# Kernel optimization log

Measured on AMD Instinct MI355X. Metric: run time of the kernel, lower is better.

The kernel has to match this reference:

```python
import jax, jax.numpy as jnp
import numpy as np

V, K, H, B = 50000, 50, 300, 512
C_WEIGHTS = 0.0005
C_TOPICS = 5e-06
BN_EPS = 1e-5


def _bn(x, g, b, m, v):
    # eval-mode BatchNorm1d with running stats
    return (x - m) * jax.lax.rsqrt(v + BN_EPS) * g + b


def setup_inputs() -> dict:
    key = jax.random.key(0)
    ks = jax.random.split(key, 16)
    s = 0.02
    inp = {
        "bows": jax.random.uniform(ks[0], (B, V), jnp.float32),
        "normalized_bows": jax.random.uniform(ks[1], (B, V), jnp.float32),
        "labels": jax.random.normal(ks[2], (B,), jnp.float32),
        # encoder q_theta: Linear(V,H) -> relu -> BN -> Linear(H,H) -> relu -> BN
        "W1": jax.random.normal(ks[3], (H, V), jnp.float32) * s,
        "b1": jnp.zeros((H,), jnp.float32),
        "W2": jax.random.normal(ks[4], (H, H), jnp.float32) * s,
        "b2": jnp.zeros((H,), jnp.float32),
        "bn1_g": jnp.ones((H,), jnp.float32),
        "bn1_b": jnp.zeros((H,), jnp.float32),
        "bn1_m": jnp.zeros((H,), jnp.float32),
        "bn1_v": jnp.ones((H,), jnp.float32),
        "bn2_g": jnp.ones((H,), jnp.float32),
        "bn2_b": jnp.zeros((H,), jnp.float32),
        "bn2_m": jnp.zeros((H,), jnp.float32),
        "bn2_v": jnp.ones((H,), jnp.float32),
        "muW": jax.random.normal(ks[5], (K, H), jnp.float32) * s,
        "mub": jnp.zeros((K,), jnp.float32),
        "lsW": jax.random.normal(ks[6], (K, H), jnp.float32) * s,
        "lsb": jnp.zeros((K,), jnp.float32),
        "logit_betas": jax.random.normal(ks[7], (V, K), jnp.float32),
        "gammas": jax.random.normal(ks[8], (V, K), jnp.float32),
        "base_rates": jax.random.normal(ks[9], (V,), jnp.float32),
        "bow_w": jax.random.normal(ks[10], (V,), jnp.float32) * s,
        "bow_b": jnp.zeros((), jnp.float32),
        "topic_w": jax.random.normal(ks[11], (K,), jnp.float32) * s,
        "topic_b": jnp.zeros((), jnp.float32),
    }
    return inp


def reference(bows, normalized_bows, labels, W1, b1, W2, b2,
              bn1_g, bn1_b, bn1_m, bn1_v, bn2_g, bn2_b, bn2_m, bn2_v,
              muW, mub, lsW, lsb, logit_betas, gammas, base_rates,
              bow_w, bow_b, topic_w, topic_b):
    # ---- encode (eval mode: reparameterize returns mu) ----
    h = _bn(jax.nn.relu(normalized_bows @ W1.T + b1), bn1_g, bn1_b, bn1_m, bn1_v)
    h = _bn(jax.nn.relu(h @ W2.T + b2), bn2_g, bn2_b, bn2_m, bn2_v)
    mu = h @ muW.T + mub                       # [B, K]
    logsigma = h @ lsW.T + lsb                 # [B, K]
    kld_theta = -0.5 * jnp.mean(jnp.sum(1.0 + logsigma - mu ** 2 - jnp.exp(logsigma), axis=-1))
    theta = jax.nn.softmax(mu, axis=-1)        # [B, K]

    # ---- decode + reconstruction loss ----
    logits = theta @ logit_betas.T + base_rates          # [B, V]
    preds = jnp.log(jax.nn.softmax(logits, axis=-1) + 1e-06)
    recon_loss = -jnp.mean(jnp.sum(preds * bows, axis=1))

    # ---- other_loss: L1 on base_rates ----
    other_loss = C_WEIGHTS * jnp.sum(jnp.abs(base_rates))

    # ---- predict_labels (hstm-all), reordered contraction: (bows @ scaled_beta) * theta
    scaled_beta = logit_betas * gammas                   # [V, K]
    het_term = jnp.sum((normalized_bows @ scaled_beta) * theta, axis=1)  # == (bows * (theta @ scaled_beta.T)).sum(1)
    expected_pred = het_term + (normalized_bows @ bow_w + bow_b) + (theta @ topic_w + topic_b)

    other_loss = other_loss + jnp.mean((expected_pred - labels) ** 2)
    other_loss = other_loss + C_TOPICS * jnp.sum(jnp.abs(gammas))
    other_loss = other_loss + C_WEIGHTS * jnp.linalg.norm(bow_w)

    return recon_loss, other_loss, kld_theta
```

## Files before the change

### kernel.cpp

```cpp
#include <hip/hip_runtime.h>
#include <hip/hip_bf16.h>
#include <math.h>


#define B_  512
#define V_  50000
#define VP  50016
#define K_  50
#define H_  300
#define KP  64
#define NW  384
#define NSTEP 1563
#define NSB  782
#define TS   8
#define NT_ST 196
#define NB_W1T (5*NT_ST)
#define NB_NBT (8*NT_ST)
#define LROW 264

typedef __attribute__((ext_vector_type(8))) short short8;
typedef __attribute__((ext_vector_type(4))) float f32x4;

typedef __attribute__((address_space(3))) void lds_void;
typedef __attribute__((address_space(1))) const void gbl_void;

static __device__ __forceinline__ void gl_lds16(const void* g, void* l) {
  __builtin_amdgcn_global_load_lds((gbl_void*)g, (lds_void*)l, 16, 0, 0);
}

static __device__ __forceinline__ short bf16s(float f) {
  unsigned int u = __builtin_bit_cast(unsigned int, f);
  u += 0x7fffu + ((u >> 16) & 1u);
  return (short)(u >> 16);
}

static __device__ __forceinline__ unsigned int pkbf(float lo, float hi) {
  __hip_bfloat162 t = __float22bfloat162_rn(float2{lo, hi});
  unsigned int u; __builtin_memcpy(&u, &t, 4); return u;
}

static __device__ __forceinline__ short8 to_bf8(float4 a, float4 b) {
  unsigned int u[4];
  u[0] = pkbf(a.x, a.y); u[1] = pkbf(a.z, a.w);
  u[2] = pkbf(b.x, b.y); u[3] = pkbf(b.z, b.w);
  short8 r; __builtin_memcpy(&r, u, 16); return r;
}

__global__ __launch_bounds__(256) void k_prep(
    const float* __restrict__ W1,
    const float* __restrict__ beta, const float* __restrict__ gamma,
    const float* __restrict__ br,   const float* __restrict__ bw,
    const float* __restrict__ nb,
    short* __restrict__ Wcatb, short* __restrict__ betab,
    short* __restrict__ nbb,
    float* __restrict__ pg, float* __restrict__ pbr, float* __restrict__ pbw2)
{
  __shared__ __attribute__((aligned(16))) char smem[64 * LROW * 4];
  const int tid = threadIdx.x;
  const short8 z8 = {0, 0, 0, 0, 0, 0, 0, 0};

  if (blockIdx.x < NB_W1T || blockIdx.x >= NB_W1T + NSB) {
    const float* src; short* dst; int r0, nrows, frame, blk;
    if (blockIdx.x < NB_W1T) {
      blk = blockIdx.x; src = W1; dst = Wcatb; frame = 12288;
      const int band = blk / NT_ST;
      r0 = band * 64; nrows = (band == 4) ? 44 : 64;
    } else {
      blk = blockIdx.x - (NB_W1T + NSB); src = nb; dst = nbb; frame = 16384;
      const int band = blk / NT_ST;
      r0 = band * 64; nrows = 64;
    }
    const int stile = blk % NT_ST;
    const int s0 = stile * TS;
    int ns = NSTEP - s0; if (ns > TS) ns = TS;

    float* ldsf = (float*)smem;
    const int wv = tid >> 6, lane = tid & 63;
    int col = s0 * 32 + lane * 4;
    if (col > V_ - 4) col = V_ - 4;
    #pragma unroll
    for (int j = 0; j < 16; ++j) {
      const int row = wv * 16 + j;
      if (row < nrows)
        gl_lds16(src + (size_t)(r0 + row) * V_ + col, ldsf + row * LROW);
    }
    asm volatile("s_waitcnt vmcnt(0)" ::: "memory");
    __syncthreads();
    const int row = tid >> 2, qo = tid & 3;
    if (row < nrows) {
      const float* lp = ldsf + row * LROW + qo * 8;
      short* dp = dst + (size_t)s0 * frame + (size_t)(r0 + row) * 32 + qo * 8;
      for (int stl = 0; stl < ns; ++stl) {
        const int kb = (s0 + stl) * 32 + qo * 8;
        short8 o = z8;
        if (kb + 8 <= V_) {
          const float* p = lp + stl * 32;
          o = to_bf8(*(const float4*)p, *(const float4*)(p + 4));
        }
        *(short8*)(dp + (size_t)stl * frame) = o;
      }
    }
    return;
  }

  short* sbt = (short*)smem;
  short* bbt = sbt + 64 * 52;
  float* redA = (float*)(smem + 13312);

  const int blk = blockIdx.x - NB_W1T;
  const int v0 = blk * 64;
  const int nvalid = (V_ - v0 < 64) ? (V_ - v0) : 64;
  const int nwrite = (VP - v0 < 64) ? (VP - v0) : 64;

  const int nf4 = (nvalid * 50) / 4;
  const float4* bsrc = (const float4*)(beta  + (size_t)v0 * 50);
  const float4* gsrc = (const float4*)(gamma + (size_t)v0 * 50);
  float gabs = 0.f;
  for (int f = tid; f < nf4; f += 256) {
    float4 bv = bsrc[f];
    float4 gv = gsrc[f];
    float be[4] = {bv.x, bv.y, bv.z, bv.w};
    float ge[4] = {gv.x, gv.y, gv.z, gv.w};
    #pragma unroll
    for (int e = 0; e < 4; ++e) {
      int idx = f * 4 + e;
      int j = idx / 50, k = idx - j * 50;
      gabs += fabsf(ge[e]);
      bbt[j * 52 + k] = bf16s(be[e]);
      sbt[j * 52 + k] = bf16s(be[e] * ge[e]);
    }
  }
  #pragma unroll
  for (int off = 1; off < 64; off <<= 1) gabs += __shfl_xor(gabs, off, 64);
  if ((tid & 63) == 0) redA[tid >> 6] = gabs;
  if (tid < 64) {
    float s1 = 0.f, s2 = 0.f;
    if (tid < nvalid) {
      s1 = fabsf(br[v0 + tid]);
      float w = bw[v0 + tid]; s2 = w * w;
    }
    #pragma unroll
    for (int off = 1; off < 64; off <<= 1) {
      s1 += __shfl_xor(s1, off, 64);
      s2 += __shfl_xor(s2, off, 64);
    }
    if (tid == 0) { pbr[blk] = s1; pbw2[blk] = s2; }
  }
  __syncthreads();
  if (tid == 0) pg[blk] = redA[0] + redA[1] + redA[2] + redA[3];

  const int j = tid & 63;
  const int q = tid >> 6;
  #pragma unroll
  for (int p = 0; p < 21; ++p) {
    const int kk = p * 4 + q;
    if (j < nwrite) {
      short val = 0;
      if (j < nvalid) {
        if (kk >= 20 && kk < 70)      val = sbt[j * 52 + (kk - 20)];
        else if (kk == 70)            val = bf16s(bw[v0 + j]);
      }
      Wcatb[(size_t)(blk * 2 + (j >> 5)) * 12288 + (300 + kk) * 32 + (j & 31)] = val;
    }
  }
  if (j < nvalid) {
    __attribute__((aligned(16))) short tmp[16];
    #pragma unroll
    for (int t = 0; t < 16; ++t) {
      int k = q * 16 + t;
      tmp[t] = (k < K_) ? bbt[j * 52 + k] : (short)0;
    }
    short8* dst = (short8*)(betab + (size_t)(v0 + j) * 64 + q * 16);
    dst[0] = *(const short8*)&tmp[0];
    dst[1] = *(const short8*)&tmp[8];
  }
}

__global__ __launch_bounds__(256, 3) void k_bg(
    const short* __restrict__ Ab, const short* __restrict__ Bb,
    float* __restrict__ part, int sps)
{
  const int t = blockIdx.x;
  const int s = t / 12;
  const int r = t % 12;
  const int bni = r % 3, bmi = r / 3;
  const int lane = threadIdx.x & 63, wv = threadIdx.x >> 6;
  const int l15 = lane & 15, quad = lane >> 4;
  const int m0 = bmi * 128 + (wv & 1) * 64;
  const int n0 = bni * 128 + (wv >> 1) * 64;
  int st0 = s * sps, st1 = st0 + sps;
  if (st0 > NSTEP) st0 = NSTEP;
  if (st1 > NSTEP) st1 = NSTEP;
  const int nst = st1 - st0;

  const short8* pa = (const short8*)Ab + (size_t)st0 * 2048 + (m0 + l15) * 4 + quad;
  const short8* pb = (const short8*)Bb + (size_t)st0 * 1536 + (n0 + l15) * 4 + quad;

  f32x4 acc[4][4];
  #pragma unroll
  for (int i = 0; i < 4; ++i)
    #pragma unroll
    for (int jj = 0; jj < 4; ++jj) acc[i][jj] = f32x4{0.f, 0.f, 0.f, 0.f};

  short8 A0[4], A1[4], B0[4], B1[4];

  auto ld = [&](short8 (&Af)[4], short8 (&Bf)[4]) {
    #pragma unroll
    for (int i = 0; i < 4; ++i) Af[i] = pa[i * 64];
    #pragma unroll
    for (int jj = 0; jj < 4; ++jj) Bf[jj] = pb[jj * 64];
    pa += 2048; pb += 1536;
  };
  auto comp = [&](short8 (&Af)[4], short8 (&Bf)[4]) {
    #pragma unroll
    for (int i = 0; i < 4; ++i)
      #pragma unroll
      for (int jj = 0; jj < 4; ++jj)
        acc[i][jj] = __builtin_amdgcn_mfma_f32_16x16x32_bf16(Af[i], Bf[jj], acc[i][jj], 0, 0, 0);
  };

  if (nst > 0) {
    ld(A0, B0);
    int k = 0;
    for (; k + 2 <= nst; k += 2) {
      ld(A1, B1);
      comp(A0, B0);
      if (k + 2 < nst) ld(A0, B0);
      comp(A1, B1);
    }
    if (k < nst) comp(A0, B0);
  }

  float* op = part + (size_t)s * (B_ * NW);
  #pragma unroll
  for (int i = 0; i < 4; ++i)
    #pragma unroll
    for (int jj = 0; jj < 4; ++jj)
      #pragma unroll
      for (int rr = 0; rr < 4; ++rr)
        op[(size_t)(m0 + 16 * i + quad * 4 + rr) * NW + (n0 + 16 * jj + l15)] = acc[i][jj][rr];
}

__global__ __launch_bounds__(320) void k_mlp(
    const float* __restrict__ part, int S,
    const float* __restrict__ b1,
    const float* __restrict__ g1, const float* __restrict__ bb1,
    const float* __restrict__ m1, const float* __restrict__ v1,
    const float* __restrict__ W2, const float* __restrict__ b2,
    const float* __restrict__ g2, const float* __restrict__ bb2,
    const float* __restrict__ m2, const float* __restrict__ v2,
    const float* __restrict__ muW, const float* __restrict__ mub,
    const float* __restrict__ lsW, const float* __restrict__ lsb,
    short* __restrict__ thetab, float* __restrict__ thetaf,
    float* __restrict__ hetmat, float* __restrict__ kldp)
{
  __shared__ __attribute__((aligned(16))) float h1s[H_];
  __shared__ __attribute__((aligned(16))) float h2s[H_];
  const int b = blockIdx.x;
  const int tid = threadIdx.x;
  const float* pb = part + (size_t)b * NW;

  if (tid < H_) {
    float s0 = 0.f, s1 = 0.f, s2 = 0.f, s3 = 0.f;
    int i = 0;
    for (; i + 4 <= S; i += 4) {
      s0 += pb[(size_t)(i + 0) * (B_ * NW) + tid];
      s1 += pb[(size_t)(i + 1) * (B_ * NW) + tid];
      s2 += pb[(size_t)(i + 2) * (B_ * NW) + tid];
      s3 += pb[(size_t)(i + 3) * (B_ * NW) + tid];
    }
    for (; i < S; ++i) s0 += pb[(size_t)i * (B_ * NW) + tid];
    float s = (s0 + s1) + (s2 + s3);
    float x = fmaxf(s + b1[tid], 0.f);
    h1s[tid] = (x - m1[tid]) * rsqrtf(v1[tid] + 1e-5f) * g1[tid] + bb1[tid];
  }
  if (tid < 51) {
    float s0 = 0.f, s1 = 0.f;
    int i = 0;
    for (; i + 2 <= S; i += 2) {
      s0 += pb[(size_t)(i + 0) * (B_ * NW) + 320 + tid];
      s1 += pb[(size_t)(i + 1) * (B_ * NW) + 320 + tid];
    }
    for (; i < S; ++i) s0 += pb[(size_t)i * (B_ * NW) + 320 + tid];
    hetmat[(size_t)b * KP + tid] = s0 + s1;
  }
  __syncthreads();
  if (tid < H_) {
    const float4* wr = (const float4*)(W2 + (size_t)tid * H_);
    const float4* hr = (const float4*)h1s;
    float acc = 0.f;
    for (int q = 0; q < H_ / 4; ++q) {
      float4 w = wr[q], h = hr[q];
      acc += w.x * h.x + w.y * h.y + w.z * h.z + w.w * h.w;
    }
    float x = fmaxf(acc + b2[tid], 0.f);
    h2s[tid] = (x - m2[tid]) * rsqrtf(v2[tid] + 1e-5f) * g2[tid] + bb2[tid];
  }
  __syncthreads();
  if (tid < 64) {
    float mu = 0.f, ls = 0.f;
    if (tid < K_) {
      const float4* mr = (const float4*)(muW + (size_t)tid * H_);
      const float4* lr = (const float4*)(lsW + (size_t)tid * H_);
      const float4* hr = (const float4*)h2s;
      for (int q = 0; q < H_ / 4; ++q) {
        float4 h = hr[q], a = mr[q], c = lr[q];
        mu += a.x * h.x + a.y * h.y + a.z * h.z + a.w * h.w;
        ls += c.x * h.x + c.y * h.y + c.z * h.z + c.w * h.w;
      }
      mu += mub[tid]; ls += lsb[tid];
    }
    float term = (tid < K_) ? (1.f + ls - mu * mu - __expf(ls)) : 0.f;
    float ts = term;
    #pragma unroll
    for (int off = 1; off < 64; off <<= 1) ts += __shfl_xor(ts, off, 64);
    if (tid == 0) kldp[b] = ts;
    float mv = (tid < K_) ? mu : -INFINITY;
    #pragma unroll
    for (int off = 1; off < 64; off <<= 1) mv = fmaxf(mv, __shfl_xor(mv, off, 64));
    float e = (tid < K_) ? __expf(mu - mv) : 0.f;
    float se = e;
    #pragma unroll
    for (int off = 1; off < 64; off <<= 1) se += __shfl_xor(se, off, 64);
    float tv = (tid < K_) ? (e / se) : 0.f;
    thetaf[(size_t)b * KP + tid] = tv;
    thetab[(size_t)b * KP + tid] = bf16s(tv);
  }
}

__global__ __launch_bounds__(256, 2) void k_c1(
    const short* __restrict__ thetab, const short* __restrict__ betab,
    const float* __restrict__ br, float* __restrict__ c1p)
{
  const int blk = blockIdx.x;
  const int bm = blk & 7, vs = blk >> 3;
  const int lane = threadIdx.x & 63, wv = threadIdx.x >> 6;
  const int l15 = lane & 15, quad = lane >> 4;
  const int b0 = bm * 64 + wv * 16;
  const short8* arow = (const short8*)(thetab + (size_t)(b0 + l15) * KP);
  const short8 a0 = arow[quad], a1 = arow[4 + quad];
  int t0 = vs * 33, t1 = t0 + 33; if (t1 > 3125) t1 = 3125;
  float p0 = 0.f, p1 = 0.f, p2 = 0.f, p3 = 0.f;
  auto body = [&](int tt) {
    const int v0 = tt * 16;
    const short8* brow = (const short8*)(betab + (size_t)(v0 + l15) * KP);
    short8 q0 = brow[quad], q1 = brow[4 + quad];
    f32x4 acc = {0.f, 0.f, 0.f, 0.f};
    acc = __builtin_amdgcn_mfma_f32_16x16x32_bf16(a0, q0, acc, 0, 0, 0);
    acc = __builtin_amdgcn_mfma_f32_16x16x32_bf16(a1, q1, acc, 0, 0, 0);
    const float brv = br[v0 + l15];
    p0 += __expf(acc[0] + brv);
    p1 += __expf(acc[1] + brv);
    p2 += __expf(acc[2] + brv);
    p3 += __expf(acc[3] + brv);
  };
  int tt = t0;
  for (; tt + 2 <= t1; tt += 2) { body(tt); body(tt + 1); }
  if (tt < t1) body(tt);
  #pragma unroll
  for (int off = 1; off < 16; off <<= 1) {
    p0 += __shfl_xor(p0, off, 16);
    p1 += __shfl_xor(p1, off, 16);
    p2 += __shfl_xor(p2, off, 16);
    p3 += __shfl_xor(p3, off, 16);
  }
  if (l15 == 0) {
    float* dst = c1p + (size_t)vs * B_ + b0 + quad * 4;
    dst[0] = p0; dst[1] = p1; dst[2] = p2; dst[3] = p3;
  }
}

static __device__ __forceinline__ float blockred512(float x, float* red) {
  #pragma unroll
  for (int off = 1; off < 64; off <<= 1) x += __shfl_xor(x, off, 64);
  if ((threadIdx.x & 63) == 0) red[threadIdx.x >> 6] = x;
  __syncthreads();
  float r = 0.f;
  if (threadIdx.x == 0)
    for (int i = 0; i < 8; ++i) r += red[i];
  __syncthreads();
  return r;
}

__global__ __launch_bounds__(512) void k_d1(
    const float* __restrict__ c1p, const float* __restrict__ kldp,
    const float* __restrict__ pg, const float* __restrict__ pbr,
    const float* __restrict__ pbw2,
    const float* __restrict__ hetmat, const float* __restrict__ thetaf,
    const float* __restrict__ labels, const float* __restrict__ topic_w,
    const float* __restrict__ topic_b, const float* __restrict__ bow_b,
    float* __restrict__ lseb, float* __restrict__ out)
{
  __shared__ float red[8];
  const int b = threadIdx.x;
  float se = 0.f;
  for (int i = 0; i < 96; ++i) se += c1p[(size_t)i * B_ + b];
  lseb[b] = __logf(se);
  float het = 0.f, tpc = 0.f;
  #pragma unroll
  for (int k = 0; k < K_; ++k) {
    float th = thetaf[(size_t)b * KP + k];
    het += th * hetmat[(size_t)b * KP + k];
    tpc += th * topic_w[k];
  }
  float ep = het + hetmat[(size_t)b * KP + 50] + bow_b[0] + tpc + topic_b[0];
  float d = ep - labels[b];
  float mse  = blockred512(d * d, red);
  float kl   = blockred512(kldp[b], red);
  float sg = 0.f, sr = 0.f, sw = 0.f;
  for (int i = b; i < NSB; i += 512) { sg += pg[i]; sr += pbr[i]; sw += pbw2[i]; }
  sg = blockred512(sg, red);
  sr = blockred512(sr, red);
  sw = blockred512(sw, red);
  if (b == 0) {
    out[1] = 0.0005f * sr + mse / (float)B_ + 5e-6f * sg + 0.0005f * sqrtf(sw);
    out[2] = -0.5f * kl / (float)B_;
  }
}

__global__ __launch_bounds__(256, 2) void k_c2(
    const short* __restrict__ thetab, const short* __restrict__ betab,
    const float* __restrict__ br, const float* __restrict__ lseb,
    const float* __restrict__ bows, float* __restrict__ c2p)
{
  __shared__ float red[4];
  const int blk = blockIdx.x;
  const int bm = blk & 7, vs = blk >> 3;
  const int lane = threadIdx.x & 63, wv = threadIdx.x >> 6;
  const int l15 = lane & 15, quad = lane >> 4;
  const int b0 = bm * 64 + wv * 16;
  const short8* arow = (const short8*)(thetab + (size_t)(b0 + l15) * KP);
  const short8 a0 = arow[quad], a1 = arow[4 + quad];
  float lse4[4]; const float* bro[4];
  #pragma unroll
  for (int rr = 0; rr < 4; ++rr) {
    lse4[rr] = lseb[b0 + quad * 4 + rr];
    bro[rr] = bows + (size_t)(b0 + quad * 4 + rr) * V_;
  }
  int t0 = vs * 33, t1 = t0 + 33; if (t1 > 3125) t1 = 3125;
  float p = 0.f;
  auto body = [&](int tt) {
    const int v0 = tt * 16;
    const int v = v0 + l15;
    const short8* brow = (const short8*)(betab + (size_t)v * KP);
    short8 q0 = brow[quad], q1 = brow[4 + quad];
    f32x4 acc = {0.f, 0.f, 0.f, 0.f};
    acc = __builtin_amdgcn_mfma_f32_16x16x32_bf16(a0, q0, acc, 0, 0, 0);
    acc = __builtin_amdgcn_mfma_f32_16x16x32_bf16(a1, q1, acc, 0, 0, 0);
    const float brv = br[v];
    #pragma unroll
    for (int rr = 0; rr < 4; ++rr) {
      float l = acc[rr] + brv - lse4[rr];
      float pr = __logf(__expf(l) + 1e-6f);
      p += pr * bro[rr][v];
    }
  };
  int tt = t0;
  for (; tt + 2 <= t1; tt += 2) { body(tt); body(tt + 1); }
  if (tt < t1) body(tt);
  #pragma unroll
  for (int off = 1; off < 64; off <<= 1) p += __shfl_xor(p, off, 64);
  if (lane == 0) red[wv] = p;
  __syncthreads();
  if (threadIdx.x == 0) c2p[blk] = red[0] + red[1] + red[2] + red[3];
}

__global__ __launch_bounds__(256) void k_d2(
    const float* __restrict__ c2p, float* __restrict__ out)
{
  __shared__ float red[4];
  float s = 0.f;
  for (int i = threadIdx.x; i < 768; i += 256) s += c2p[i];
  #pragma unroll
  for (int off = 1; off < 64; off <<= 1) s += __shfl_xor(s, off, 64);
  if ((threadIdx.x & 63) == 0) red[threadIdx.x >> 6] = s;
  __syncthreads();
  if (threadIdx.x == 0)
    out[0] = -(red[0] + red[1] + red[2] + red[3]) / (float)B_;
}

extern "C" void kernel_launch(void* const* d_in, const int* in_sizes, int n_in,
                              void* d_out, int out_size, void* d_ws, size_t ws_size,
                              hipStream_t stream)
{
  const float* bows    = (const float*)d_in[0];
  const float* nb      = (const float*)d_in[1];
  const float* labels  = (const float*)d_in[2];
  const float* W1      = (const float*)d_in[3];
  const float* b1      = (const float*)d_in[4];
  const float* W2      = (const float*)d_in[5];
  const float* b2      = (const float*)d_in[6];
  const float* bn1_g   = (const float*)d_in[7];
  const float* bn1_b   = (const float*)d_in[8];
  const float* bn1_m   = (const float*)d_in[9];
  const float* bn1_v   = (const float*)d_in[10];
  const float* bn2_g   = (const float*)d_in[11];
  const float* bn2_b   = (const float*)d_in[12];
  const float* bn2_m   = (const float*)d_in[13];
  const float* bn2_v   = (const float*)d_in[14];
  const float* muW     = (const float*)d_in[15];
  const float* mub     = (const float*)d_in[16];
  const float* lsW     = (const float*)d_in[17];
  const float* lsb     = (const float*)d_in[18];
  const float* beta    = (const float*)d_in[19];
  const float* gamma   = (const float*)d_in[20];
  const float* brates  = (const float*)d_in[21];
  const float* bow_w   = (const float*)d_in[22];
  const float* bow_b   = (const float*)d_in[23];
  const float* topic_w = (const float*)d_in[24];
  const float* topic_b = (const float*)d_in[25];
  float* out = (float*)d_out;

  char* ws = (char*)d_ws;
  size_t off = 0;
  auto take = [&](size_t bytes) { void* p = ws + off; off = (off + bytes + 255) & ~(size_t)255; return p; };

  short* Wcatb   = (short*)take((size_t)NSTEP * 12288 * 2);
  short* nbb     = (short*)take((size_t)NSTEP * 16384 * 2);
  short* betab   = (short*)take((size_t)V_ * 64 * 2);
  short* thetab  = (short*)take((size_t)B_ * KP * 2);
  float* thetaf  = (float*)take((size_t)B_ * KP * 4);
  float* hetmat  = (float*)take((size_t)B_ * KP * 4);
  float* kldp    = (float*)take((size_t)B_ * 4);
  float* c1p     = (float*)take((size_t)96 * B_ * 4);
  float* c2p     = (float*)take((size_t)768 * 4);
  float* lse_    = (float*)take((size_t)B_ * 4);
  float* pg      = (float*)take((size_t)NSB * 4);
  float* pbr     = (float*)take((size_t)NSB * 4);
  float* pbw2    = (float*)take((size_t)NSB * 4);
  float* part1   = (float*)(ws + off);
  size_t remain = (ws_size > off) ? (ws_size - off) : 0;
  int S = (int)(remain / ((size_t)B_ * NW * 4));
  if (S > 64) S = 64;
  if (S < 1)  S = 1;
  const int sps = (NSTEP + S - 1) / S;

  k_prep<<<NB_W1T + NSB + NB_NBT, 256, 0, stream>>>(
      W1, beta, gamma, brates, bow_w, nb, Wcatb, betab, nbb, pg, pbr, pbw2);
  k_bg  <<<12 * S, 256, 0, stream>>>(nbb, Wcatb, part1, sps);
  k_mlp <<<B_, 320, 0, stream>>>(part1, S, b1, bn1_g, bn1_b, bn1_m, bn1_v,
                                 W2, b2, bn2_g, bn2_b, bn2_m, bn2_v,
                                 muW, mub, lsW, lsb, thetab, thetaf, hetmat, kldp);
  k_c1  <<<8 * 96, 256, 0, stream>>>(thetab, betab, brates, c1p);
  k_d1  <<<1, 512, 0, stream>>>(c1p, kldp, pg, pbr, pbw2, hetmat, thetaf,
                                labels, topic_w, topic_b, bow_b, lse_, out);
  k_c2  <<<8 * 96, 256, 0, stream>>>(thetab, betab, brates, lse_, bows, c2p);
  k_d2  <<<1, 256, 0, stream>>>(c2p, out);
}
```

Before: 476.0 us.

## Fuse decode kernels into one with grid-wide atomic barriers; reorder prep and bg blocks

Merges k_c1, k_d1, k_c2 and k_d2 into a single k_cde kernel. Atomic counters elect the last-arriving block to do the reductions, and the other blocks spin until it publishes lse, which removes three kernel launches and their inter-kernel gaps. It also moves the normalized_bows conversion tiles to the front of k_prep and changes k_bg so consecutive blocks cover the same output tile across K-splits. The spin barrier depends on all 768 blocks being resident at once (launch_bounds 3 per CU), and a failed co-residency would deadlock.

```diff
diff --git a/kernel.cpp b/kernel.cpp
--- a/kernel.cpp
+++ b/kernel.cpp
@@ -46,6 +46,48 @@
   short8 r; __builtin_memcpy(&r, u, 16); return r;
 }
 
+static __device__ __forceinline__ void cvt_tile_body(
+    char* smem, const float* __restrict__ src, short* __restrict__ dst,
+    int blk, int frame, int nrows_last_band, int nbands_last)
+{
+  const int tid = threadIdx.x;
+  const short8 z8 = {0, 0, 0, 0, 0, 0, 0, 0};
+
+  const int band = blk / NT_ST;
+  const int r0 = band * 64;
+  const int nrows = (band == nbands_last) ? nrows_last_band : 64;
+  const int stile = blk % NT_ST;
+  const int s0 = stile * TS;
+  int ns = NSTEP - s0; if (ns > TS) ns = TS;
+
+  float* ldsf = (float*)smem;
+  const int wv = tid >> 6, lane = tid & 63;
+  int col = s0 * 32 + lane * 4;
+  if (col > V_ - 4) col = V_ - 4;
+  #pragma unroll
+  for (int j = 0; j < 16; ++j) {
+    const int row = wv * 16 + j;
+    if (row < nrows)
+      gl_lds16(src + (size_t)(r0 + row) * V_ + col, ldsf + row * LROW);
+  }
+  asm volatile("s_waitcnt vmcnt(0)" ::: "memory");
+  __syncthreads();
+  const int row = tid >> 2, qo = tid & 3;
+  if (row < nrows) {
+    const float* lp = ldsf + row * LROW + qo * 8;
+    short* dp = dst + (size_t)s0 * frame + (size_t)(r0 + row) * 32 + qo * 8;
+    for (int stl = 0; stl < ns; ++stl) {
+      const int kb = (s0 + stl) * 32 + qo * 8;
+      short8 o = z8;
+      if (kb + 8 <= V_) {
+        const float* p = lp + stl * 32;
+        o = to_bf8(*(const float4*)p, *(const float4*)(p + 4));
+      }
+      *(short8*)(dp + (size_t)stl * frame) = o;
+    }
+  }
+}
+
 __global__ __launch_bounds__(256) void k_prep(
     const float* __restrict__ W1,
     const float* __restrict__ beta, const float* __restrict__ gamma,
@@ -57,57 +99,21 @@
 {
   __shared__ __attribute__((aligned(16))) char smem[64 * LROW * 4];
   const int tid = threadIdx.x;
-  const short8 z8 = {0, 0, 0, 0, 0, 0, 0, 0};
-
-  if (blockIdx.x < NB_W1T || blockIdx.x >= NB_W1T + NSB) {
-    const float* src; short* dst; int r0, nrows, frame, blk;
-    if (blockIdx.x < NB_W1T) {
-      blk = blockIdx.x; src = W1; dst = Wcatb; frame = 12288;
-      const int band = blk / NT_ST;
-      r0 = band * 64; nrows = (band == 4) ? 44 : 64;
-    } else {
-      blk = blockIdx.x - (NB_W1T + NSB); src = nb; dst = nbb; frame = 16384;
-      const int band = blk / NT_ST;
-      r0 = band * 64; nrows = 64;
-    }
-    const int stile = blk % NT_ST;
-    const int s0 = stile * TS;
-    int ns = NSTEP - s0; if (ns > TS) ns = TS;
-
-    float* ldsf = (float*)smem;
-    const int wv = tid >> 6, lane = tid & 63;
-    int col = s0 * 32 + lane * 4;
-    if (col > V_ - 4) col = V_ - 4;
-    #pragma unroll
-    for (int j = 0; j < 16; ++j) {
-      const int row = wv * 16 + j;
-      if (row < nrows)
-        gl_lds16(src + (size_t)(r0 + row) * V_ + col, ldsf + row * LROW);
-    }
-    asm volatile("s_waitcnt vmcnt(0)" ::: "memory");
-    __syncthreads();
-    const int row = tid >> 2, qo = tid & 3;
-    if (row < nrows) {
-      const float* lp = ldsf + row * LROW + qo * 8;
-      short* dp = dst + (size_t)s0 * frame + (size_t)(r0 + row) * 32 + qo * 8;
-      for (int stl = 0; stl < ns; ++stl) {
-        const int kb = (s0 + stl) * 32 + qo * 8;
-        short8 o = z8;
-        if (kb + 8 <= V_) {
-          const float* p = lp + stl * 32;
-          o = to_bf8(*(const float4*)p, *(const float4*)(p + 4));
-        }
-        *(short8*)(dp + (size_t)stl * frame) = o;
-      }
-    }
+
+  if (blockIdx.x < NB_NBT) {
+    cvt_tile_body(smem, nb, nbb, blockIdx.x, 16384, 64, 8);
+    return;
+  }
+  if (blockIdx.x < NB_NBT + NB_W1T) {
+    cvt_tile_body(smem, W1, Wcatb, blockIdx.x - NB_NBT, 12288, 44, 4);
     return;
   }
 
   short* sbt = (short*)smem;
   short* bbt = sbt + 64 * 52;
-  float* redA = (float*)(smem + 13312);
-
-  const int blk = blockIdx.x - NB_W1T;
+  float* redA = (float*)(smem + 16384);
+
+  const int blk = blockIdx.x - (NB_NBT + NB_W1T);
   const int v0 = blk * 64;
   const int nvalid = (V_ - v0 < 64) ? (V_ - v0) : 64;
   const int nwrite = (VP - v0 < 64) ? (VP - v0) : 64;
@@ -180,9 +186,9 @@
     const short* __restrict__ Ab, const short* __restrict__ Bb,
     float* __restrict__ part, int sps)
 {
-  const int t = blockIdx.x;
-  const int s = t / 12;
-  const int r = t % 12;
+  const int S = gridDim.x / 12;
+  const int s = blockIdx.x % S;
+  const int r = blockIdx.x / S;
   const int bni = r % 3, bmi = r / 3;
   const int lane = threadIdx.x & 63, wv = threadIdx.x >> 6;
   const int l15 = lane & 15, quad = lane >> 4;
@@ -252,13 +258,16 @@
     const float* __restrict__ muW, const float* __restrict__ mub,
     const float* __restrict__ lsW, const float* __restrict__ lsb,
     short* __restrict__ thetab, float* __restrict__ thetaf,
-    float* __restrict__ hetmat, float* __restrict__ kldp)
+    float* __restrict__ hetmat, float* __restrict__ kldp,
+    unsigned int* __restrict__ syncv)
 {
   __shared__ __attribute__((aligned(16))) float h1s[H_];
   __shared__ __attribute__((aligned(16))) float h2s[H_];
   const int b = blockIdx.x;
   const int tid = threadIdx.x;
   const float* pb = part + (size_t)b * NW;
+
+  if (b == 0 && tid == 0) { syncv[0] = 0u; syncv[16] = 0u; syncv[32] = 0u; }
 
   if (tid < H_) {
     float s0 = 0.f, s1 = 0.f, s2 = 0.f, s3 = 0.f;
@@ -328,155 +337,175 @@
   }
 }
 
-__global__ __launch_bounds__(256, 2) void k_c1(
+__global__ __launch_bounds__(256, 3) void k_cde(
     const short* __restrict__ thetab, const short* __restrict__ betab,
-    const float* __restrict__ br, float* __restrict__ c1p)
+    const float* __restrict__ br, const float* __restrict__ bows,
+    const float* __restrict__ kldp,
+    const float* __restrict__ pg, const float* __restrict__ pbr,
+    const float* __restrict__ pbw2,
+    const float* __restrict__ hetmat, const float* __restrict__ thetaf,
+    const float* __restrict__ labels, const float* __restrict__ topic_w,
+    const float* __restrict__ topic_b, const float* __restrict__ bow_b,
+    float* __restrict__ c1p, float* __restrict__ c2p,
+    float* __restrict__ lseb, unsigned int* __restrict__ syncv,
+    float* __restrict__ out)
 {
-  const int blk = blockIdx.x;
-  const int bm = blk & 7, vs = blk >> 3;
-  const int lane = threadIdx.x & 63, wv = threadIdx.x >> 6;
+  __shared__ float red8[8];
+  __shared__ unsigned int lastS;
+  const int tid = threadIdx.x;
+  const int bm = blockIdx.x / 96, vs = blockIdx.x % 96;
+  const int lane = tid & 63, wv = tid >> 6;
   const int l15 = lane & 15, quad = lane >> 4;
   const int b0 = bm * 64 + wv * 16;
   const short8* arow = (const short8*)(thetab + (size_t)(b0 + l15) * KP);
   const short8 a0 = arow[quad], a1 = arow[4 + quad];
   int t0 = vs * 33, t1 = t0 + 33; if (t1 > 3125) t1 = 3125;
-  float p0 = 0.f, p1 = 0.f, p2 = 0.f, p3 = 0.f;
-  auto body = [&](int tt) {
-    const int v0 = tt * 16;
-    const short8* brow = (const short8*)(betab + (size_t)(v0 + l15) * KP);
-    short8 q0 = brow[quad], q1 = brow[4 + quad];
-    f32x4 acc = {0.f, 0.f, 0.f, 0.f};
-    acc = __builtin_amdgcn_mfma_f32_16x16x32_bf16(a0, q0, acc, 0, 0, 0);
-    acc = __builtin_amdgcn_mfma_f32_16x16x32_bf16(a1, q1, acc, 0, 0, 0);
-    const float brv = br[v0 + l15];
-    p0 += __expf(acc[0] + brv);
-    p1 += __expf(acc[1] + brv);
-    p2 += __expf(acc[2] + brv);
-    p3 += __expf(acc[3] + brv);
+
+  auto wtree = [&](float x) {
+    #pragma unroll
+    for (int off = 1; off < 64; off <<= 1) x += __shfl_xor(x, off, 64);
+    return x;
   };
-  int tt = t0;
-  for (; tt + 2 <= t1; tt += 2) { body(tt); body(tt + 1); }
-  if (tt < t1) body(tt);
-  #pragma unroll
-  for (int off = 1; off < 16; off <<= 1) {
-    p0 += __shfl_xor(p0, off, 16);
-    p1 += __shfl_xor(p1, off, 16);
-    p2 += __shfl_xor(p2, off, 16);
-    p3 += __shfl_xor(p3, off, 16);
-  }
-  if (l15 == 0) {
-    float* dst = c1p + (size_t)vs * B_ + b0 + quad * 4;
-    dst[0] = p0; dst[1] = p1; dst[2] = p2; dst[3] = p3;
-  }
-}
-
-static __device__ __forceinline__ float blockred512(float x, float* red) {
-  #pragma unroll
-  for (int off = 1; off < 64; off <<= 1) x += __shfl_xor(x, off, 64);
-  if ((threadIdx.x & 63) == 0) red[threadIdx.x >> 6] = x;
-  __syncthreads();
-  float r = 0.f;
-  if (threadIdx.x == 0)
-    for (int i = 0; i < 8; ++i) r += red[i];
-  __syncthreads();
-  return r;
-}
-
-__global__ __launch_bounds__(512) void k_d1(
-    const float* __restrict__ c1p, const float* __restrict__ kldp,
-    const float* __restrict__ pg, const float* __restrict__ pbr,
-    const float* __restrict__ pbw2,
-    const float* __restrict__ hetmat, const float* __restrict__ thetaf,
-    const float* __restrict__ labels, const float* __restrict__ topic_w,
-    const float* __restrict__ topic_b, const float* __restrict__ bow_b,
-    float* __restrict__ lseb, float* __restrict__ out)
-{
-  __shared__ float red[8];
-  const int b = threadIdx.x;
-  float se = 0.f;
-  for (int i = 0; i < 96; ++i) se += c1p[(size_t)i * B_ + b];
-  lseb[b] = __logf(se);
-  float het = 0.f, tpc = 0.f;
-  #pragma unroll
-  for (int k = 0; k < K_; ++k) {
-    float th = thetaf[(size_t)b * KP + k];
-    het += th * hetmat[(size_t)b * KP + k];
-    tpc += th * topic_w[k];
-  }
-  float ep = het + hetmat[(size_t)b * KP + 50] + bow_b[0] + tpc + topic_b[0];
-  float d = ep - labels[b];
-  float mse  = blockred512(d * d, red);
-  float kl   = blockred512(kldp[b], red);
-  float sg = 0.f, sr = 0.f, sw = 0.f;
-  for (int i = b; i < NSB; i += 512) { sg += pg[i]; sr += pbr[i]; sw += pbw2[i]; }
-  sg = blockred512(sg, red);
-  sr = blockred512(sr, red);
-  sw = blockred512(sw, red);
-  if (b == 0) {
-    out[1] = 0.0005f * sr + mse / (float)B_ + 5e-6f * sg + 0.0005f * sqrtf(sw);
-    out[2] = -0.5f * kl / (float)B_;
-  }
-}
-
-__global__ __launch_bounds__(256, 2) void k_c2(
-    const short* __restrict__ thetab, const short* __restrict__ betab,
-    const float* __restrict__ br, const float* __restrict__ lseb,
-    const float* __restrict__ bows, float* __restrict__ c2p)
-{
-  __shared__ float red[4];
-  const int blk = blockIdx.x;
-  const int bm = blk & 7, vs = blk >> 3;
-  const int lane = threadIdx.x & 63, wv = threadIdx.x >> 6;
-  const int l15 = lane & 15, quad = lane >> 4;
-  const int b0 = bm * 64 + wv * 16;
-  const short8* arow = (const short8*)(thetab + (size_t)(b0 + l15) * KP);
-  const short8 a0 = arow[quad], a1 = arow[4 + quad];
-  float lse4[4]; const float* bro[4];
-  #pragma unroll
-  for (int rr = 0; rr < 4; ++rr) {
-    lse4[rr] = lseb[b0 + quad * 4 + rr];
-    bro[rr] = bows + (size_t)(b0 + quad * 4 + rr) * V_;
-  }
-  int t0 = vs * 33, t1 = t0 + 33; if (t1 > 3125) t1 = 3125;
-  float p = 0.f;
-  auto body = [&](int tt) {
-    const int v0 = tt * 16;
-    const int v = v0 + l15;
-    const short8* brow = (const short8*)(betab + (size_t)v * KP);
-    short8 q0 = brow[quad], q1 = brow[4 + quad];
-    f32x4 acc = {0.f, 0.f, 0.f, 0.f};
-    acc = __builtin_amdgcn_mfma_f32_16x16x32_bf16(a0, q0, acc, 0, 0, 0);
-    acc = __builtin_amdgcn_mfma_f32_16x16x32_bf16(a1, q1, acc, 0, 0, 0);
-    const float brv = br[v];
+
+  {
+    float p0 = 0.f, p1 = 0.f, p2 = 0.f, p3 = 0.f;
+    auto body = [&](int tt) {
+      const int v0 = tt * 16;
+      const short8* brow = (const short8*)(betab + (size_t)(v0 + l15) * KP);
+      short8 q0 = brow[quad], q1 = brow[4 + quad];
+      f32x4 acc = {0.f, 0.f, 0.f, 0.f};
+      acc = __builtin_amdgcn_mfma_f32_16x16x32_bf16(a0, q0, acc, 0, 0, 0);
+      acc = __builtin_amdgcn_mfma_f32_16x16x32_bf16(a1, q1, acc, 0, 0, 0);
+      const float brv = br[v0 + l15];
+      p0 += __expf(acc[0] + brv);
+      p1 += __expf(acc[1] + brv);
+      p2 += __expf(acc[2] + brv);
+      p3 += __expf(acc[3] + brv);
+    };
+    int tt = t0;
+    for (; tt + 2 <= t1; tt += 2) { body(tt); body(tt + 1); }
+    if (tt < t1) body(tt);
+    #pragma unroll
+    for (int off = 1; off < 16; off <<= 1) {
+      p0 += __shfl_xor(p0, off, 16);
+      p1 += __shfl_xor(p1, off, 16);
+      p2 += __shfl_xor(p2, off, 16);
+      p3 += __shfl_xor(p3, off, 16);
+    }
+    if (l15 == 0) {
+      float* dst = c1p + (size_t)vs * B_ + b0 + quad * 4;
+      dst[0] = p0; dst[1] = p1; dst[2] = p2; dst[3] = p3;
+    }
+  }
+
+  __threadfence();
+  __syncthreads();
+  if (tid == 0) lastS = (atomicAdd(&syncv[0], 1u) == 767u) ? 1u : 0u;
+  __syncthreads();
+
+  if (lastS) {
+    float dd[2], kv[2], sgv[2], srv[2], swv[2];
+    #pragma unroll 2
+    for (int ph = 0; ph < 2; ++ph) {
+      const int b = tid + ph * 256;
+      float se = 0.f;
+      for (int i = 0; i < 96; ++i) se += c1p[(size_t)i * B_ + b];
+      lseb[b] = __logf(se);
+      float het = 0.f, tpc = 0.f;
+      #pragma unroll
+      for (int k = 0; k < K_; ++k) {
+        float th = thetaf[(size_t)b * KP + k];
+        het += th * hetmat[(size_t)b * KP + k];
+        tpc += th * topic_w[k];
+      }
+      float ep = het + hetmat[(size_t)b * KP + 50] + bow_b[0] + tpc + topic_b[0];
+      float d = ep - labels[b];
+      dd[ph] = d * d;
+      kv[ph] = kldp[b];
+      float sg = 0.f, sr = 0.f, sw = 0.f;
+      for (int i = b; i < NSB; i += 512) { sg += pg[i]; sr += pbr[i]; sw += pbw2[i]; }
+      sgv[ph] = sg; srv[ph] = sr; swv[ph] = sw;
+    }
+    auto bred = [&](float xA, float xB) {
+      float tA = wtree(xA), tB = wtree(xB);
+      if (lane == 0) { red8[wv] = tA; red8[4 + wv] = tB; }
+      __syncthreads();
+      float r = 0.f;
+      if (tid == 0) for (int i = 0; i < 8; ++i) r += red8[i];
+      __syncthreads();
+      return r;
+    };
+    float mse = bred(dd[0], dd[1]);
+    float kl  = bred(kv[0], kv[1]);
+    float sg  = bred(sgv[0], sgv[1]);
+    float sr  = bred(srv[0], srv[1]);
+    float sw  = bred(swv[0], swv[1]);
+    if (tid == 0) {
+      out[1] = 0.0005f * sr + mse / (float)B_ + 5e-6f * sg + 0.0005f * sqrtf(sw);
+      out[2] = -0.5f * kl / (float)B_;
+    }
+    __threadfence();
+    __syncthreads();
+    if (tid == 0)
+      __hip_atomic_store(&syncv[16], 1u, __ATOMIC_RELEASE, __HIP_MEMORY_SCOPE_AGENT);
+  } else {
+    if (tid == 0) {
+      while (__hip_atomic_load(&syncv[16], __ATOMIC_ACQUIRE,
+                               __HIP_MEMORY_SCOPE_AGENT) == 0u)
+        __builtin_amdgcn_s_sleep(8);
+    }
+    __syncthreads();
+  }
+
+  {
+    float lse4[4]; const float* bro[4];
     #pragma unroll
     for (int rr = 0; rr < 4; ++rr) {
-      float l = acc[rr] + brv - lse4[rr];
-      float pr = __logf(__expf(l) + 1e-6f);
-      p += pr * bro[rr][v];
-    }
-  };
-  int tt = t0;
-  for (; tt + 2 <= t1; tt += 2) { body(tt); body(tt + 1); }
-  if (tt < t1) body(tt);
-  #pragma unroll
-  for (int off = 1; off < 64; off <<= 1) p += __shfl_xor(p, off, 64);
-  if (lane == 0) red[wv] = p;
-  __syncthreads();
-  if (threadIdx.x == 0) c2p[blk] = red[0] + red[1] + red[2] + red[3];
-}
-
-__global__ __launch_bounds__(256) void k_d2(
-    const float* __restrict__ c2p, float* __restrict__ out)
-{
-  __shared__ float red[4];
-  float s = 0.f;
-  for (int i = threadIdx.x; i < 768; i += 256) s += c2p[i];
-  #pragma unroll
-  for (int off = 1; off < 64; off <<= 1) s += __shfl_xor(s, off, 64);
-  if ((threadIdx.x & 63) == 0) red[threadIdx.x >> 6] = s;
-  __syncthreads();
-  if (threadIdx.x == 0)
-    out[0] = -(red[0] + red[1] + red[2] + red[3]) / (float)B_;
+      lse4[rr] = __hip_atomic_load(lseb + (b0 + quad * 4 + rr),
+                                   __ATOMIC_RELAXED, __HIP_MEMORY_SCOPE_AGENT);
+      bro[rr] = bows + (size_t)(b0 + quad * 4 + rr) * V_;
+    }
+    float p = 0.f;
+    auto body = [&](int tt) {
+      const int v0 = tt * 16;
+      const int v = v0 + l15;
+      const short8* brow = (const short8*)(betab + (size_t)v * KP);
+      short8 q0 = brow[quad], q1 = brow[4 + quad];
+      f32x4 acc = {0.f, 0.f, 0.f, 0.f};
+      acc = __builtin_amdgcn_mfma_f32_16x16x32_bf16(a0, q0, acc, 0, 0, 0);
+      acc = __builtin_amdgcn_mfma_f32_16x16x32_bf16(a1, q1, acc, 0, 0, 0);
+      const float brv = br[v];
+      #pragma unroll
+      for (int rr = 0; rr < 4; ++rr) {
+        float l = acc[rr] + brv - lse4[rr];
+        float pr = __logf(__expf(l) + 1e-6f);
+        p += pr * bro[rr][v];
+      }
+    };
+    int tt = t0;
+    for (; tt + 2 <= t1; tt += 2) { body(tt); body(tt + 1); }
+    if (tt < t1) body(tt);
+    p = wtree(p);
+    if (lane == 0) red8[wv] = p;
+    __syncthreads();
+    if (tid == 0) c2p[(size_t)vs * 8 + bm] = red8[0] + red8[1] + red8[2] + red8[3];
+  }
+
+  __threadfence();
+  __syncthreads();
+  if (tid == 0) lastS = (atomicAdd(&syncv[32], 1u) == 767u) ? 1u : 0u;
+  __syncthreads();
+
+  if (lastS) {
+    float s = 0.f;
+    for (int i = tid; i < 768; i += 256)
+      s += __hip_atomic_load(&c2p[i], __ATOMIC_RELAXED, __HIP_MEMORY_SCOPE_AGENT);
+    s = wtree(s);
+    if (lane == 0) red8[wv] = s;
+    __syncthreads();
+    if (tid == 0)
+      out[0] = -(red8[0] + red8[1] + red8[2] + red8[3]) / (float)B_;
+  }
 }
 
 extern "C" void kernel_launch(void* const* d_in, const int* in_sizes, int n_in,
@@ -528,6 +557,7 @@
   float* pg      = (float*)take((size_t)NSB * 4);
   float* pbr     = (float*)take((size_t)NSB * 4);
   float* pbw2    = (float*)take((size_t)NSB * 4);
+  unsigned int* syncv = (unsigned int*)take(256);
   float* part1   = (float*)(ws + off);
   size_t remain = (ws_size > off) ? (ws_size - off) : 0;
   int S = (int)(remain / ((size_t)B_ * NW * 4));
@@ -535,15 +565,15 @@
   if (S < 1)  S = 1;
   const int sps = (NSTEP + S - 1) / S;
 
-  k_prep<<<NB_W1T + NSB + NB_NBT, 256, 0, stream>>>(
+  k_prep<<<NB_NBT + NB_W1T + NSB, 256, 0, stream>>>(
       W1, beta, gamma, brates, bow_w, nb, Wcatb, betab, nbb, pg, pbr, pbw2);
   k_bg  <<<12 * S, 256, 0, stream>>>(nbb, Wcatb, part1, sps);
   k_mlp <<<B_, 320, 0, stream>>>(part1, S, b1, bn1_g, bn1_b, bn1_m, bn1_v,
                                  W2, b2, bn2_g, bn2_b, bn2_m, bn2_v,
-                                 muW, mub, lsW, lsb, thetab, thetaf, hetmat, kldp);
-  k_c1  <<<8 * 96, 256, 0, stream>>>(thetab, betab, brates, c1p);
-  k_d1  <<<1, 512, 0, stream>>>(c1p, kldp, pg, pbr, pbw2, hetmat, thetaf,
-                                labels, topic_w, topic_b, bow_b, lse_, out);
-  k_c2  <<<8 * 96, 256, 0, stream>>>(thetab, betab, brates, lse_, bows, c2p);
-  k_d2  <<<1, 256, 0, stream>>>(c2p, out);
-}
+                                 muW, mub, lsW, lsb, thetab, thetaf, hetmat, kldp,
+                                 syncv);
+  k_cde <<<8 * 96, 256, 0, stream>>>(thetab, betab, brates, bows, kldp,
+                                     pg, pbr, pbw2, hetmat, thetaf, labels,
+                                     topic_w, topic_b, bow_b,
+                                     c1p, c2p, lse_, syncv, out);
+}
```

Result: slower. 867.1 us (+82.1%).
